# Kernel tuning notes

Hardware: AMD Instinct MI355X
Metric: run time of the kernel (lower is better)

Reference implementation:

```python
import jax, jax.numpy as jnp
import numpy as np

NUM_HEADS = 16


def setup_inputs() -> dict:
    key = jax.random.key(0)
    ks = jax.random.split(key, 5)
    b, s, d = 2, 2048, 1024
    std = (2.0 / (d + d)) ** 0.5
    x = jax.random.normal(ks[0], (b, s, d), dtype=jnp.float32)
    Wq = jax.random.normal(ks[1], (d, d), dtype=jnp.float32) * std
    Wk = jax.random.normal(ks[2], (d, d), dtype=jnp.float32) * std
    Wv = jax.random.normal(ks[3], (d, d), dtype=jnp.float32) * std
    Wo = jax.random.normal(ks[4], (d, d), dtype=jnp.float32) * std
    return {"x": x, "Wq": Wq, "Wk": Wk, "Wv": Wv, "Wo": Wo}


def reference(x, Wq, Wk, Wv, Wo):
    b, s, d = x.shape
    h = NUM_HEADS
    dk = d // h
    # projections: bias-free x @ W (W is [in, out])
    def split_heads(t):
        return t.reshape(b, s, h, dk).transpose(0, 2, 1, 3)  # b h s dk
    q = split_heads(x @ Wq)
    k = split_heads(x @ Wk)
    v = split_heads(x @ Wv)
    scale = 1.0 / jnp.sqrt(jnp.asarray(dk, dtype=x.dtype))
    scores = jnp.einsum('bhqd,bhkd->bhqk', q, k) * scale  # b h s s
    causal = jnp.tril(jnp.ones((s, s), dtype=bool))
    scores = jnp.where(causal, scores, -jnp.inf)
    probs = jax.nn.softmax(scores, axis=-1)
    out = jnp.einsum('bhqk,bhkd->bhqd', probs, v)
    out = out.transpose(0, 2, 1, 3).reshape(b, s, d)  # b s (h dk)
    return out @ Wo
```

## Files before the change

### kernel.cpp

```cpp
#include <hip/hip_runtime.h>

typedef unsigned short u16;
typedef unsigned int   u32;

using bf16x8 = __attribute__((ext_vector_type(8))) __bf16;
using bf16x4 = __attribute__((ext_vector_type(4))) __bf16;
using f32x4  = __attribute__((ext_vector_type(4))) float;
using s16x4  = __attribute__((ext_vector_type(4))) short;

#define NH    16
#define DKH   64
#define SEQ   2048
#define BAT   2
#define DMOD  1024

#define QSCALE 0.18033688011112042f

__device__ __forceinline__ u16 f2bf(float f) {
  union { float f; u32 u; } v; v.f = f;
  u32 r = v.u + 0x7fffu + ((v.u >> 16) & 1u);
  return (u16)(r >> 16);
}

__device__ __forceinline__ u32 pack2bf(float a, float b) {
  union { float f; u32 u; } x, y; x.f = a; y.f = b;
  u32 ua = x.u + 0x7fffu + ((x.u >> 16) & 1u);
  u32 ub = y.u + 0x7fffu + ((y.u >> 16) & 1u);
  return __builtin_amdgcn_perm(ub, ua, 0x07060302u);
}

__device__ __forceinline__ s16x4 pk4bf(float a, float b, float c, float d) {
  union { bf16x4 bv; s16x4 sv; } u;
  u.bv[0] = (__bf16)a; u.bv[1] = (__bf16)b; u.bv[2] = (__bf16)c; u.bv[3] = (__bf16)d;
  return u.sv;
}

#if __has_builtin(__builtin_amdgcn_exp2f)
#define EXP2(x) __builtin_amdgcn_exp2f(x)
#else
#define EXP2(x) exp2f(x)
#endif

#if __has_builtin(__builtin_amdgcn_mfma_f32_16x16x16bf16_1k)
__device__ __forceinline__ f32x4 mfma16(s16x4 a, s16x4 b, f32x4 c) {
  return __builtin_amdgcn_mfma_f32_16x16x16bf16_1k(a, b, c, 0, 0, 0);
}
#else
__device__ __forceinline__ f32x4 mfma16(s16x4 a, s16x4 b, f32x4 c) {
  f32x4 d;
  asm volatile("v_mfma_f32_16x16x16_bf16 %0, %1, %2, %3\n\ts_nop 7\n\ts_nop 7"
               : "=v"(d) : "v"(a), "v"(b), "v"(c));
  return d;
}
#endif

typedef const __attribute__((address_space(1))) u32 glb_u32;
typedef __attribute__((address_space(3))) u32 lds_u32;
__device__ __forceinline__ void gload16(const u16* g, u16* l) {
  __builtin_amdgcn_global_load_lds((glb_u32*)(const void*)g, (lds_u32*)(void*)l, 16, 0, 0);
}

__global__ __launch_bounds__(256) void prep(const float* __restrict__ Wq,
                                            const float* __restrict__ Wk,
                                            const float* __restrict__ Wv,
                                            const float* __restrict__ Wo,
                                            u16* __restrict__ Wt,
                                            const float* __restrict__ x,
                                            u16* __restrict__ xb) {
  const int z = blockIdx.z;
  if (z < 4) {
    __shared__ u16 t[32][33];
    const float* W = z == 0 ? Wq : z == 1 ? Wk : z == 2 ? Wv : Wo;
    u16* o = Wt + (size_t)z * DMOD * DMOD;
    int bx = blockIdx.x * 32, by = blockIdx.y * 32;
    int tx = threadIdx.x, ty = threadIdx.y;
    #pragma unroll
    for (int i = 0; i < 32; i += 8)
      t[ty + i][tx] = f2bf(W[(size_t)(by + ty + i) * DMOD + bx + tx]);
    __syncthreads();
    #pragma unroll
    for (int i = 0; i < 32; i += 8)
      o[(size_t)(bx + ty + i) * DMOD + by + tx] = t[tx][ty + i];
  } else {
    int cid = blockIdx.x + 32 * blockIdx.y;
    int tid1 = threadIdx.y * 32 + threadIdx.x;
    size_t i = ((size_t)cid * 256 + tid1) * 16;
    #pragma unroll
    for (int half = 0; half < 2; ++half) {
      float4 f0 = *(const float4*)(x + i + half * 8);
      float4 f1 = *(const float4*)(x + i + half * 8 + 4);
      uint4 o;
      o.x = pack2bf(f0.x, f0.y); o.y = pack2bf(f0.z, f0.w);
      o.z = pack2bf(f1.x, f1.y); o.w = pack2bf(f1.z, f1.w);
      *(uint4*)(xb + i + half * 8) = o;
    }
  }
}

__global__ __launch_bounds__(256, 3) void gemm_qkv(const u16* __restrict__ A,
                                                   const u16* __restrict__ Bt,
                                                   u16* __restrict__ Qo,
                                                   u16* __restrict__ Ko,
                                                   u16* __restrict__ Vo) {
  __shared__ __align__(16) u16 As[128 * 64];
  __shared__ __align__(16) u16 Bs[128 * 64];
  const int tid  = threadIdx.x;
  const int lane = tid & 63, wv = tid >> 6;
  const int wm   = wv >> 1, wn = wv & 1;
  const int lrow = lane & 15, quad = lane >> 4;
  const int tileM = blockIdx.x * 128, tileN = blockIdx.y * 128;

  const f32x4 fz = {0.f, 0.f, 0.f, 0.f};
  f32x4 acc[4][4];
  #pragma unroll
  for (int i = 0; i < 4; ++i)
    #pragma unroll
    for (int j = 0; j < 4; ++j) acc[i][j] = fz;

  for (int kt = 0; kt < DMOD; kt += 64) {
    if (kt) __syncthreads();
    #pragma unroll
    for (int i = 0; i < 4; ++i) {
      int idx = i * 256 + tid;
      int r = idx >> 3, c = idx & 7;
      gload16(&A [(size_t)(tileM + r) * DMOD + kt + ((c ^ (r & 7)) << 3)], &As[idx * 8]);
      gload16(&Bt[(size_t)(tileN + r) * DMOD + kt + ((c ^ (r & 7)) << 3)], &Bs[idx * 8]);
    }
    __syncthreads();

    #pragma unroll
    for (int kk = 0; kk < 2; ++kk) {
      bf16x8 af[4], bfr[4];
      #pragma unroll
      for (int mt = 0; mt < 4; ++mt)
        af[mt] = *(const bf16x8*)(&As[(wm * 64 + mt * 16 + lrow) * 64
                                      + (((kk * 4 + quad) ^ (lrow & 7)) << 3)]);
      #pragma unroll
      for (int nt = 0; nt < 4; ++nt)
        bfr[nt] = *(const bf16x8*)(&Bs[(wn * 64 + nt * 16 + lrow) * 64
                                       + (((kk * 4 + quad) ^ (lrow & 7)) << 3)]);
      #pragma unroll
      for (int mt = 0; mt < 4; ++mt)
        #pragma unroll
        for (int nt = 0; nt < 4; ++nt)
          acc[mt][nt] = __builtin_amdgcn_mfma_f32_16x16x32_bf16(af[mt], bfr[nt],
                                                                acc[mt][nt], 0, 0, 0);
    }
  }

  #pragma unroll
  for (int mt = 0; mt < 4; ++mt) {
    #pragma unroll
    for (int nt = 0; nt < 4; ++nt) {
      int gm0 = tileM + wm * 64 + mt * 16 + quad * 4;
      int gn  = tileN + wn * 64 + nt * 16 + lrow;
      int which = gn >> 10, col = gn & 1023;
      int bb = gm0 >> 11, srw0 = gm0 & (SEQ - 1);
      int hh = col >> 6, dki = col & (DKH - 1);
      size_t bhi = (size_t)(bb * NH + hh);
      if (which == 0) {
        #pragma unroll
        for (int r = 0; r < 4; ++r)
          Qo[(bhi * SEQ + srw0 + r) * DKH + dki] = f2bf(acc[mt][nt][r] * QSCALE);
      } else if (which == 1) {
        #pragma unroll
        for (int r = 0; r < 4; ++r)
          Ko[(bhi * SEQ + srw0 + r) * DKH + dki] = f2bf(acc[mt][nt][r]);
      } else {
        uint2 pk;
        pk.x = pack2bf(acc[mt][nt][0], acc[mt][nt][1]);
        pk.y = pack2bf(acc[mt][nt][2], acc[mt][nt][3]);
        *(uint2*)(&Vo[(((bhi * (SEQ / 4)) + (srw0 >> 2)) * DKH + dki) * 4]) = pk;
      }
    }
  }
}

__global__ __launch_bounds__(256, 3) void gemm_out(const u16* __restrict__ A,
                                                   const u16* __restrict__ Bt,
                                                   float* __restrict__ Co) {
  __shared__ __align__(16) u16 As[128 * 64];
  __shared__ __align__(16) u16 Bs[64 * 64];
  const int tid  = threadIdx.x;
  const int lane = tid & 63, wv = tid >> 6;
  const int wm   = wv & 1, wn = wv >> 1;
  const int lrow = lane & 15, quad = lane >> 4;
  const int tileM = blockIdx.x * 128, tileN = blockIdx.y * 64;

  const f32x4 fz = {0.f, 0.f, 0.f, 0.f};
  f32x4 acc[4][2];
  #pragma unroll
  for (int i = 0; i < 4; ++i) { acc[i][0] = fz; acc[i][1] = fz; }

  for (int kt = 0; kt < DMOD; kt += 64) {
    if (kt) __syncthreads();
    #pragma unroll
    for (int i = 0; i < 4; ++i) {
      int idx = i * 256 + tid;
      int r = idx >> 3, c = idx & 7;
      gload16(&A[(size_t)(tileM + r) * DMOD + kt + ((c ^ (r & 7)) << 3)], &As[idx * 8]);
    }
    #pragma unroll
    for (int i = 0; i < 2; ++i) {
      int idx = i * 256 + tid;
      int r = idx >> 3, c = idx & 7;
      gload16(&Bt[(size_t)(tileN + r) * DMOD + kt + ((c ^ (r & 7)) << 3)], &Bs[idx * 8]);
    }
    __syncthreads();

    #pragma unroll
    for (int kk = 0; kk < 2; ++kk) {
      bf16x8 af[4], bfr[2];
      #pragma unroll
      for (int mt = 0; mt < 4; ++mt)
        af[mt] = *(const bf16x8*)(&As[(wm * 64 + mt * 16 + lrow) * 64
                                      + (((kk * 4 + quad) ^ (lrow & 7)) << 3)]);
      #pragma unroll
      for (int nt = 0; nt < 2; ++nt)
        bfr[nt] = *(const bf16x8*)(&Bs[(wn * 32 + nt * 16 + lrow) * 64
                                       + (((kk * 4 + quad) ^ (lrow & 7)) << 3)]);
      #pragma unroll
      for (int mt = 0; mt < 4; ++mt)
        #pragma unroll
        for (int nt = 0; nt < 2; ++nt)
          acc[mt][nt] = __builtin_amdgcn_mfma_f32_16x16x32_bf16(af[mt], bfr[nt],
                                                                acc[mt][nt], 0, 0, 0);
    }
  }

  #pragma unroll
  for (int mt = 0; mt < 4; ++mt)
    #pragma unroll
    for (int nt = 0; nt < 2; ++nt)
      #pragma unroll
      for (int r = 0; r < 4; ++r) {
        int gm = tileM + wm * 64 + mt * 16 + quad * 4 + r;
        int gn = tileN + wn * 32 + nt * 16 + lrow;
        Co[(size_t)gm * DMOD + gn] = acc[mt][nt][r];
      }
}

#define OPAD 68

__global__ __launch_bounds__(256, 2) void attn_k(const u16* __restrict__ Q,
                                                 const u16* __restrict__ Kg,
                                                 const u16* __restrict__ Vg,
                                                 u16* __restrict__ Og) {
  __shared__ __align__(16) u16 Ksb[2][2][64 * 64];
  __shared__ __align__(16) u16 Vsb[2][2][16 * 256];
  __shared__ __align__(16) u16 Osc[64 * OPAD];
  __shared__ float Lsc[32];

  const int tid  = threadIdx.x;
  const int lane = tid & 63, w = tid >> 6;
  const int g    = w >> 1,  wg = w & 1;
  const int lrow = lane & 15, quad = lane >> 4;
  const int bh = blockIdx.x, y = blockIdx.y;
  const int b = bh >> 4, h = bh & 15;
  const int qB = 31 - y;
  const int sAend = y >> 1;

  const u16* Qbh = Q  + (size_t)bh * SEQ * DKH;
  const u16* Kbh = Kg + (size_t)bh * SEQ * DKH;
  const u16* Vbh = Vg + (size_t)bh * SEQ * DKH;

  const f32x4 fz = {0.f, 0.f, 0.f, 0.f};
  f32x4 oacc[2][4];
  float lsum[2];
  bf16x8 bq[2][2];

#define DEC(s_, g_, qt_, j_, v_)                                                   \
  { if ((s_) <= sAend) { qt_ = y;  j_ = 2 * (s_) + (g_);              v_ = (j_ <= y);  } \
    else               { qt_ = qB; j_ = 2 * ((s_) - sAend - 1) + (g_); v_ = (j_ <= qB); } }

#define STAGE1(gg, p_, j_)                                                          \
  { _Pragma("unroll")                                                               \
    for (int i_ = 0; i_ < 2; ++i_) {                                                \
      int cD = i_ * 256 + tid; int r_ = cD >> 3, c_ = cD & 7;                       \
      gload16(&Kbh[(size_t)((j_) * 64 + r_) * DKH + ((c_ ^ (r_ & 7)) << 3)],        \
              &Ksb[gg][p_][cD * 8]); }                                              \
    _Pragma("unroll")                                                               \
    for (int i_ = 0; i_ < 2; ++i_) {                                                \
      int cD = i_ * 256 + tid; int sq_ = cD >> 5, c_ = cD & 31;                     \
      gload16(&Vbh[(size_t)((j_) * 16 + sq_) * 256 + ((c_ ^ (sq_ & 7)) << 3)],      \
              &Vsb[gg][p_][cD * 8]); } }

#define LOADQ(qt_)                                                                  \
  { _Pragma("unroll")                                                               \
    for (int s_ = 0; s_ < 2; ++s_)                                                  \
      _Pragma("unroll")                                                             \
      for (int kk_ = 0; kk_ < 2; ++kk_)                                             \
        bq[s_][kk_] = *(const bf16x8*)(&Qbh[(size_t)((qt_) * 64 + wg * 32 + s_ * 16 \
                                            + lrow) * DKH + kk_ * 32 + quad * 8]); }

  auto EPI = [&](int qt) {
    float ls[2];
    #pragma unroll
    for (int s2 = 0; s2 < 2; ++s2) {
      float v = lsum[s2];
      v += __shfl_xor(v, 16, 64);
      v += __shfl_xor(v, 32, 64);
      ls[s2] = v;
    }
    float* OscF = (float*)Osc;
    #pragma unroll
    for (int ph = 0; ph < 2; ++ph) {
      if (g == 1) {
        int srow = wg * 16 + lrow;
        #pragma unroll
        for (int d = 0; d < 4; ++d)
          *(f32x4*)(&OscF[srow * OPAD + d * 16 + quad * 4]) = oacc[ph][d];
        if (quad == 0) Lsc[srow] = ls[ph];
      }
      __syncthreads();
      if (g == 0) {
        int srow = wg * 16 + lrow;
        ls[ph] += Lsc[srow];
        #pragma unroll
        for (int d = 0; d < 4; ++d) {
          f32x4 ov = *(const f32x4*)(&OscF[srow * OPAD + d * 16 + quad * 4]);
          oacc[ph][d] += ov;
        }
      }
      __syncthreads();
    }
    if (g == 0) {
      #pragma unroll
      for (int s2 = 0; s2 < 2; ++s2) {
        float inv = 1.f / ls[s2];
        int row = wg * 32 + s2 * 16 + lrow;
        #pragma unroll
        for (int d = 0; d < 4; ++d) {
          uint2 pkk;
          pkk.x = pack2bf(oacc[s2][d][0] * inv, oacc[s2][d][1] * inv);
          pkk.y = pack2bf(oacc[s2][d][2] * inv, oacc[s2][d][3] * inv);
          *(uint2*)(&Osc[row * OPAD + d * 16 + quad * 4]) = pkk;
        }
      }
    }
    __syncthreads();
    #pragma unroll
    for (int k2 = 0; k2 < 2; ++k2) {
      int c2 = k2 * 256 + tid;
      int row = c2 >> 3, ch = c2 & 7;
      uint4 vv = *(const uint4*)(&Osc[row * OPAD + ch * 8]);
      *(uint4*)(&Og[(size_t)(b * SEQ + qt * 64 + row) * DMOD + h * DKH + ch * 8]) = vv;
    }
  };

  { int qt0, j0; bool v0;
    DEC(0, 0, qt0, j0, v0); if (v0) STAGE1(0, 0, j0);
    DEC(0, 1, qt0, j0, v0); if (v0) STAGE1(1, 0, j0);
  }
  LOADQ(y);
  #pragma unroll
  for (int s2 = 0; s2 < 2; ++s2) {
    oacc[s2][0] = fz; oacc[s2][1] = fz; oacc[s2][2] = fz; oacc[s2][3] = fz;
    lsum[s2] = 0.f;
  }
  __syncthreads();

  for (int s = 0; s <= 16; ++s) {
    const int p = s & 1;

    if (s < 16) {
      int qtn, jn; bool vn;
      DEC(s + 1, 0, qtn, jn, vn); if (vn) STAGE1(0, p ^ 1, jn);
      DEC(s + 1, 1, qtn, jn, vn); if (vn) STAGE1(1, p ^ 1, jn);
    }

    int qt, j; bool valid;
    DEC(s, g, qt, j, valid);
    if (valid) {
      const u16* Ks = Ksb[g][p];
      const u16* Vs = Vsb[g][p];
      if (j < qt) {
        __builtin_amdgcn_s_setprio(1);
        f32x4 sacc[2][4];
        #pragma unroll
        for (int s2 = 0; s2 < 2; ++s2)
          #pragma unroll
          for (int m = 0; m < 4; ++m) sacc[s2][m] = fz;
        #pragma unroll
        for (int kk = 0; kk < 2; ++kk)
          #pragma unroll
          for (int m = 0; m < 4; ++m) {
            bf16x8 ak = *(const bf16x8*)(&Ks[(m * 16 + lrow) * 64
                                             + (((kk * 4 + quad) ^ (lrow & 7)) << 3)]);
            sacc[0][m] = __builtin_amdgcn_mfma_f32_16x16x32_bf16(ak, bq[0][kk], sacc[0][m], 0, 0, 0);
            sacc[1][m] = __builtin_amdgcn_mfma_f32_16x16x32_bf16(ak, bq[1][kk], sacc[1][m], 0, 0, 0);
          }
        #pragma unroll
        for (int m = 0; m < 4; ++m) {
          float p00 = EXP2(sacc[0][m][0]), p01 = EXP2(sacc[0][m][1]);
          float p02 = EXP2(sacc[0][m][2]), p03 = EXP2(sacc[0][m][3]);
          float p10 = EXP2(sacc[1][m][0]), p11 = EXP2(sacc[1][m][1]);
          float p12 = EXP2(sacc[1][m][2]), p13 = EXP2(sacc[1][m][3]);
          lsum[0] += (p00 + p01) + (p02 + p03);
          lsum[1] += (p10 + p11) + (p12 + p13);
          s16x4 pk0 = pk4bf(p00, p01, p02, p03);
          s16x4 pk1 = pk4bf(p10, p11, p12, p13);
          const int sq = m * 4 + quad;
          #pragma unroll
          for (int d = 0; d < 4; ++d) {
            int dk = d * 16 + lrow;
            s16x4 av = *(const s16x4*)(&Vs[sq * 256
                                           + ((((dk >> 1) ^ (sq & 7)) << 3) | ((dk & 1) << 2))]);
            oacc[0][d] = mfma16(av, pk0, oacc[0][d]);
            oacc[1][d] = mfma16(av, pk1, oacc[1][d]);
          }
        }
        __builtin_amdgcn_s_setprio(0);
      } else {
        #pragma unroll
        for (int s2 = 0; s2 < 2; ++s2) {
          const int L = 2 * wg + s2;
          for (int m = 0; m < L; ++m) {
            f32x4 sv = fz;
            #pragma unroll
            for (int kk = 0; kk < 2; ++kk) {
              bf16x8 ak = *(const bf16x8*)(&Ks[(m * 16 + lrow) * 64
                                               + (((kk * 4 + quad) ^ (lrow & 7)) << 3)]);
              sv = __builtin_amdgcn_mfma_f32_16x16x32_bf16(ak, bq[s2][kk], sv, 0, 0, 0);
            }
            float p0 = EXP2(sv[0]), p1 = EXP2(sv[1]), p2 = EXP2(sv[2]), p3 = EXP2(sv[3]);
            lsum[s2] += (p0 + p1) + (p2 + p3);
            s16x4 pk = pk4bf(p0, p1, p2, p3);
            const int sq = m * 4 + quad;
            #pragma unroll
            for (int d = 0; d < 4; ++d) {
              int dk = d * 16 + lrow;
              s16x4 av = *(const s16x4*)(&Vs[sq * 256
                                             + ((((dk >> 1) ^ (sq & 7)) << 3) | ((dk & 1) << 2))]);
              oacc[s2][d] = mfma16(av, pk, oacc[s2][d]);
            }
          }
          {
            f32x4 sv = fz;
            #pragma unroll
            for (int kk = 0; kk < 2; ++kk) {
              bf16x8 ak = *(const bf16x8*)(&Ks[(L * 16 + lrow) * 64
                                               + (((kk * 4 + quad) ^ (lrow & 7)) << 3)]);
              sv = __builtin_amdgcn_mfma_f32_16x16x32_bf16(ak, bq[s2][kk], sv, 0, 0, 0);
            }
            float pp[4];
            #pragma unroll
            for (int r = 0; r < 4; ++r)
              pp[r] = (quad * 4 + r > lrow) ? 0.f : EXP2(sv[r]);
            lsum[s2] += (pp[0] + pp[1]) + (pp[2] + pp[3]);
            s16x4 pk = pk4bf(pp[0], pp[1], pp[2], pp[3]);
            const int sq = L * 4 + quad;
            #pragma unroll
            for (int d = 0; d < 4; ++d) {
              int dk = d * 16 + lrow;
              s16x4 av = *(const s16x4*)(&Vs[sq * 256
                                             + ((((dk >> 1) ^ (sq & 7)) << 3) | ((dk & 1) << 2))]);
              oacc[s2][d] = mfma16(av, pk, oacc[s2][d]);
            }
          }
        }
      }
    }

    __syncthreads();

    if (s == sAend) {
      EPI(y);
      #pragma unroll
      for (int s2 = 0; s2 < 2; ++s2) {
        oacc[s2][0] = fz; oacc[s2][1] = fz; oacc[s2][2] = fz; oacc[s2][3] = fz;
        lsum[s2] = 0.f;
      }
      LOADQ(qB);
    } else if (s == 16) {
      EPI(qB);
    }
  }
#undef DEC
#undef STAGE1
#undef LOADQ
}

extern "C" void kernel_launch(void* const* d_in, const int* in_sizes, int n_in,
                              void* d_out, int out_size, void* d_ws, size_t ws_size,
                              hipStream_t stream) {
  const float* x  = (const float*)d_in[0];
  const float* Wq = (const float*)d_in[1];
  const float* Wk = (const float*)d_in[2];
  const float* Wv = (const float*)d_in[3];
  const float* Wo = (const float*)d_in[4];

  u16* ws = (u16*)d_ws;
  const size_t WSZ = (size_t)DMOD * DMOD;
  const size_t TSZ = (size_t)BAT * NH * SEQ * DKH;
  u16* Wt  = ws;
  u16* Wto = Wt + 3 * WSZ;
  u16* xb  = Wt + 4 * WSZ;
  u16* Qb  = xb + TSZ;
  u16* Kb  = Qb + TSZ;
  u16* Vb  = Kb + TSZ;
  u16* Ob  = xb;

  prep<<<dim3(32, 32, 5), dim3(32, 8), 0, stream>>>(Wq, Wk, Wv, Wo, Wt, x, xb);

  gemm_qkv<<<dim3(32, 24), 256, 0, stream>>>(xb, Wt, Qb, Kb, Vb);

  attn_k<<<dim3(32, 16), 256, 0, stream>>>(Qb, Kb, Vb, Ob);

  gemm_out<<<dim3(32, 16), 256, 0, stream>>>(Ob, Wto, (float*)d_out);
}
```

Measured before the change: 159.7 us.

## Split attention KV work across four wave groups with 32-key tiles

The attention kernel now runs 512 threads per block, with four wave groups each taking 32-key chunks of the KV sequence instead of two groups each taking 64-key chunks. Partial outputs are reduced across the four groups through shared memory in the epilogue, and the causal diagonal handling is redone at the 32-key granularity. The goal is more parallel waves per query tile, which gives better latency hiding and load balance. The cost is a longer reduction epilogue with more barriers and more synchronization per step.

```diff
diff --git a/kernel.cpp b/kernel.cpp
--- a/kernel.cpp
+++ b/kernel.cpp
@@ -242,14 +242,14 @@
 
 #define OPAD 68
 
-__global__ __launch_bounds__(256, 2) void attn_k(const u16* __restrict__ Q,
+__global__ __launch_bounds__(512, 4) void attn_k(const u16* __restrict__ Q,
                                                  const u16* __restrict__ Kg,
                                                  const u16* __restrict__ Vg,
                                                  u16* __restrict__ Og) {
-  __shared__ __align__(16) u16 Ksb[2][2][64 * 64];
-  __shared__ __align__(16) u16 Vsb[2][2][16 * 256];
+  __shared__ __align__(16) u16 Ksb[4][2][32 * 64];
+  __shared__ __align__(16) u16 Vsb[4][2][8 * 256];
   __shared__ __align__(16) u16 Osc[64 * OPAD];
-  __shared__ float Lsc[32];
+  __shared__ float Lsc4[64 * 4];
 
   const int tid  = threadIdx.x;
   const int lane = tid & 63, w = tid >> 6;
@@ -269,21 +269,29 @@
   float lsum[2];
   bf16x8 bq[2][2];
 
-#define DEC(s_, g_, qt_, j_, v_)                                                   \
-  { if ((s_) <= sAend) { qt_ = y;  j_ = 2 * (s_) + (g_);              v_ = (j_ <= y);  } \
-    else               { qt_ = qB; j_ = 2 * ((s_) - sAend - 1) + (g_); v_ = (j_ <= qB); } }
-
-#define STAGE1(gg, p_, j_)                                                          \
-  { _Pragma("unroll")                                                               \
-    for (int i_ = 0; i_ < 2; ++i_) {                                                \
-      int cD = i_ * 256 + tid; int r_ = cD >> 3, c_ = cD & 7;                       \
-      gload16(&Kbh[(size_t)((j_) * 64 + r_) * DKH + ((c_ ^ (r_ & 7)) << 3)],        \
-              &Ksb[gg][p_][cD * 8]); }                                              \
-    _Pragma("unroll")                                                               \
-    for (int i_ = 0; i_ < 2; ++i_) {                                                \
-      int cD = i_ * 256 + tid; int sq_ = cD >> 5, c_ = cD & 31;                     \
-      gload16(&Vbh[(size_t)((j_) * 16 + sq_) * 256 + ((c_ ^ (sq_ & 7)) << 3)],      \
-              &Vsb[gg][p_][cD * 8]); } }
+#define DEC(s_, g_, qt_, j_, v_)                                                    \
+  { if ((s_) <= sAend) { qt_ = y;  j_ = 4 * (s_) + (g_);              v_ = (j_ <= 2 * y + 1); } \
+    else               { qt_ = qB; j_ = 4 * ((s_) - sAend - 1) + (g_); v_ = (j_ <= 2 * qB + 1); } }
+
+#define STAGE4(p_, s_)                                                              \
+  { int qt_, j_; bool v_;                                                           \
+    const int gi = tid >> 7;                                                        \
+    DEC(s_, gi, qt_, j_, v_); (void)qt_;                                            \
+    if (v_) {                                                                       \
+      const int ci = tid & 127;                                                     \
+      _Pragma("unroll")                                                             \
+      for (int i_ = 0; i_ < 2; ++i_) {                                              \
+        int ch = i_ * 128 + ci; int r_ = ch >> 3, c_ = ch & 7;                      \
+        gload16(&Kbh[(size_t)(j_ * 32 + r_) * DKH + ((c_ ^ (r_ & 7)) << 3)],        \
+                &Ksb[gi][p_][ch * 8]);                                              \
+      }                                                                             \
+      _Pragma("unroll")                                                             \
+      for (int i_ = 0; i_ < 2; ++i_) {                                              \
+        int ch = i_ * 128 + ci; int sq_ = ch >> 5, c_ = ch & 31;                    \
+        gload16(&Vbh[(size_t)(j_ * 8 + sq_) * 256 + ((c_ ^ (sq_ & 7)) << 3)],       \
+                &Vsb[gi][p_][ch * 8]);                                              \
+      }                                                                             \
+    } }
 
 #define LOADQ(qt_)                                                                  \
   { _Pragma("unroll")                                                               \
@@ -302,32 +310,46 @@
       v += __shfl_xor(v, 32, 64);
       ls[s2] = v;
     }
+    if (quad == 0) {
+      Lsc4[(wg * 32 + lrow) * 4 + g]      = ls[0];
+      Lsc4[(wg * 32 + 16 + lrow) * 4 + g] = ls[1];
+    }
+    __syncthreads();
+    float lt[2];
+    #pragma unroll
+    for (int s2 = 0; s2 < 2; ++s2) {
+      int row = wg * 32 + s2 * 16 + lrow;
+      lt[s2] = (Lsc4[row * 4 + 0] + Lsc4[row * 4 + 1])
+             + (Lsc4[row * 4 + 2] + Lsc4[row * 4 + 3]);
+    }
     float* OscF = (float*)Osc;
-    #pragma unroll
-    for (int ph = 0; ph < 2; ++ph) {
-      if (g == 1) {
-        int srow = wg * 16 + lrow;
-        #pragma unroll
-        for (int d = 0; d < 4; ++d)
-          *(f32x4*)(&OscF[srow * OPAD + d * 16 + quad * 4]) = oacc[ph][d];
-        if (quad == 0) Lsc[srow] = ls[ph];
+    for (int pg = 1; pg <= 3; ++pg) {
+      #pragma unroll
+      for (int ph = 0; ph < 2; ++ph) {
+        if (g == pg && wg == ph) {
+          #pragma unroll
+          for (int s2 = 0; s2 < 2; ++s2)
+            #pragma unroll
+            for (int d = 0; d < 4; ++d)
+              *(f32x4*)(&OscF[(s2 * 16 + lrow) * OPAD + d * 16 + quad * 4]) = oacc[s2][d];
+        }
+        __syncthreads();
+        if (g == 0 && wg == ph) {
+          #pragma unroll
+          for (int s2 = 0; s2 < 2; ++s2)
+            #pragma unroll
+            for (int d = 0; d < 4; ++d) {
+              f32x4 ov = *(const f32x4*)(&OscF[(s2 * 16 + lrow) * OPAD + d * 16 + quad * 4]);
+              oacc[s2][d] += ov;
+            }
+        }
+        __syncthreads();
       }
-      __syncthreads();
-      if (g == 0) {
-        int srow = wg * 16 + lrow;
-        ls[ph] += Lsc[srow];
-        #pragma unroll
-        for (int d = 0; d < 4; ++d) {
-          f32x4 ov = *(const f32x4*)(&OscF[srow * OPAD + d * 16 + quad * 4]);
-          oacc[ph][d] += ov;
-        }
-      }
-      __syncthreads();
     }
     if (g == 0) {
       #pragma unroll
       for (int s2 = 0; s2 < 2; ++s2) {
-        float inv = 1.f / ls[s2];
+        float inv = 1.f / lt[s2];
         int row = wg * 32 + s2 * 16 + lrow;
         #pragma unroll
         for (int d = 0; d < 4; ++d) {
@@ -339,19 +361,14 @@
       }
     }
     __syncthreads();
-    #pragma unroll
-    for (int k2 = 0; k2 < 2; ++k2) {
-      int c2 = k2 * 256 + tid;
-      int row = c2 >> 3, ch = c2 & 7;
+    {
+      int row = tid >> 3, ch = tid & 7;
       uint4 vv = *(const uint4*)(&Osc[row * OPAD + ch * 8]);
       *(uint4*)(&Og[(size_t)(b * SEQ + qt * 64 + row) * DMOD + h * DKH + ch * 8]) = vv;
     }
   };
 
-  { int qt0, j0; bool v0;
-    DEC(0, 0, qt0, j0, v0); if (v0) STAGE1(0, 0, j0);
-    DEC(0, 1, qt0, j0, v0); if (v0) STAGE1(1, 0, j0);
-  }
+  STAGE4(0, 0);
   LOADQ(y);
   #pragma unroll
   for (int s2 = 0; s2 < 2; ++s2) {
@@ -363,35 +380,29 @@
   for (int s = 0; s <= 16; ++s) {
     const int p = s & 1;
 
-    if (s < 16) {
-      int qtn, jn; bool vn;
-      DEC(s + 1, 0, qtn, jn, vn); if (vn) STAGE1(0, p ^ 1, jn);
-      DEC(s + 1, 1, qtn, jn, vn); if (vn) STAGE1(1, p ^ 1, jn);
-    }
+    if (s < 16) STAGE4(p ^ 1, s + 1);
 
     int qt, j; bool valid;
     DEC(s, g, qt, j, valid);
     if (valid) {
       const u16* Ks = Ksb[g][p];
       const u16* Vs = Vsb[g][p];
-      if (j < qt) {
+      const int dt = j - 2 * qt;
+      if (dt < 0 || wg > dt) {
         __builtin_amdgcn_s_setprio(1);
-        f32x4 sacc[2][4];
-        #pragma unroll
-        for (int s2 = 0; s2 < 2; ++s2)
-          #pragma unroll
-          for (int m = 0; m < 4; ++m) sacc[s2][m] = fz;
+        f32x4 sacc[2][2];
+        sacc[0][0] = fz; sacc[0][1] = fz; sacc[1][0] = fz; sacc[1][1] = fz;
         #pragma unroll
         for (int kk = 0; kk < 2; ++kk)
           #pragma unroll
-          for (int m = 0; m < 4; ++m) {
+          for (int m = 0; m < 2; ++m) {
             bf16x8 ak = *(const bf16x8*)(&Ks[(m * 16 + lrow) * 64
                                              + (((kk * 4 + quad) ^ (lrow & 7)) << 3)]);
             sacc[0][m] = __builtin_amdgcn_mfma_f32_16x16x32_bf16(ak, bq[0][kk], sacc[0][m], 0, 0, 0);
             sacc[1][m] = __builtin_amdgcn_mfma_f32_16x16x32_bf16(ak, bq[1][kk], sacc[1][m], 0, 0, 0);
           }
         #pragma unroll
-        for (int m = 0; m < 4; ++m) {
+        for (int m = 0; m < 2; ++m) {
           float p00 = EXP2(sacc[0][m][0]), p01 = EXP2(sacc[0][m][1]);
           float p02 = EXP2(sacc[0][m][2]), p03 = EXP2(sacc[0][m][3]);
           float p10 = EXP2(sacc[1][m][0]), p11 = EXP2(sacc[1][m][1]);
@@ -411,11 +422,10 @@
           }
         }
         __builtin_amdgcn_s_setprio(0);
-      } else {
+      } else if (wg == dt) {
         #pragma unroll
         for (int s2 = 0; s2 < 2; ++s2) {
-          const int L = 2 * wg + s2;
-          for (int m = 0; m < L; ++m) {
+          for (int m = 0; m <= s2; ++m) {
             f32x4 sv = fz;
             #pragma unroll
             for (int kk = 0; kk < 2; ++kk) {
@@ -423,33 +433,18 @@
                                                + (((kk * 4 + quad) ^ (lrow & 7)) << 3)]);
               sv = __builtin_amdgcn_mfma_f32_16x16x32_bf16(ak, bq[s2][kk], sv, 0, 0, 0);
             }
-            float p0 = EXP2(sv[0]), p1 = EXP2(sv[1]), p2 = EXP2(sv[2]), p3 = EXP2(sv[3]);
-            lsum[s2] += (p0 + p1) + (p2 + p3);
-            s16x4 pk = pk4bf(p0, p1, p2, p3);
-            const int sq = m * 4 + quad;
-            #pragma unroll
-            for (int d = 0; d < 4; ++d) {
-              int dk = d * 16 + lrow;
-              s16x4 av = *(const s16x4*)(&Vs[sq * 256
-                                             + ((((dk >> 1) ^ (sq & 7)) << 3) | ((dk & 1) << 2))]);
-              oacc[s2][d] = mfma16(av, pk, oacc[s2][d]);
+            float pp[4];
+            if (m == s2) {
+              #pragma unroll
+              for (int r = 0; r < 4; ++r)
+                pp[r] = (quad * 4 + r > lrow) ? 0.f : EXP2(sv[r]);
+            } else {
+              #pragma unroll
+              for (int r = 0; r < 4; ++r) pp[r] = EXP2(sv[r]);
             }
-          }
-          {
-            f32x4 sv = fz;
-            #pragma unroll
-            for (int kk = 0; kk < 2; ++kk) {
-              bf16x8 ak = *(const bf16x8*)(&Ks[(L * 16 + lrow) * 64
-                                               + (((kk * 4 + quad) ^ (lrow & 7)) << 3)]);
-              sv = __builtin_amdgcn_mfma_f32_16x16x32_bf16(ak, bq[s2][kk], sv, 0, 0, 0);
-            }
-            float pp[4];
-            #pragma unroll
-            for (int r = 0; r < 4; ++r)
-              pp[r] = (quad * 4 + r > lrow) ? 0.f : EXP2(sv[r]);
             lsum[s2] += (pp[0] + pp[1]) + (pp[2] + pp[3]);
             s16x4 pk = pk4bf(pp[0], pp[1], pp[2], pp[3]);
-            const int sq = L * 4 + quad;
+            const int sq = m * 4 + quad;
             #pragma unroll
             for (int d = 0; d < 4; ++d) {
               int dk = d * 16 + lrow;
@@ -477,7 +472,7 @@
     }
   }
 #undef DEC
-#undef STAGE1
+#undef STAGE4
 #undef LOADQ
 }
 
@@ -505,7 +500,7 @@
 
   gemm_qkv<<<dim3(32, 24), 256, 0, stream>>>(xb, Wt, Qb, Kb, Vb);
 
-  attn_k<<<dim3(32, 16), 256, 0, stream>>>(Qb, Kb, Vb, Ob);
+  attn_k<<<dim3(32, 16), 512, 0, stream>>>(Qb, Kb, Vb, Ob);
 
   gemm_out<<<dim3(32, 16), 256, 0, stream>>>(Ob, Wto, (float*)d_out);
 }
```

Measured after the change: 196.1 us. +22.8%, slower.
